# Optimization experiments

Measured on AMD Instinct MI355X. Metric: run time of the kernel, lower is better.

The kernel has to match this reference:

```python
import jax, jax.numpy as jnp
import numpy as np

N_NODES = 50000
N_EDGES = 800000
D_IN = 512
D_OUT = 512


def setup_inputs() -> dict:
    key = jax.random.key(0)
    k1, k2, k3, k4, k5 = jax.random.split(key, 5)
    x = jax.random.normal(k1, (N_NODES, D_IN), dtype=jnp.float32)
    # DGL GraphConv weight: [in_feats, out_feats], xavier-ish scale
    weight = jax.random.normal(k2, (D_IN, D_OUT), dtype=jnp.float32) * (1.0 / np.sqrt(D_IN))
    bias = jax.random.normal(k3, (D_OUT,), dtype=jnp.float32) * 0.01
    src = jax.random.randint(k4, (N_EDGES,), 0, N_NODES, dtype=jnp.int64)
    dst = jax.random.randint(k5, (N_EDGES,), 0, N_NODES, dtype=jnp.int64)
    return {"x": x, "weight": weight, "bias": bias, "src": src, "dst": dst}


def reference(x, weight, bias, src, dst):
    # DGL GraphConv with norm='none': sum messages from src -> dst, then linear.
    # (in_feats == out_feats so DGL aggregates first, then applies W; math is
    # identical either way.)
    msgs = x[src]                                            # [E, D_IN] gather
    agg = jax.ops.segment_sum(msgs, dst, num_segments=N_NODES)  # [N, D_IN]
    return agg @ weight + bias                               # [N, D_OUT]
```

## Files before the change

kernel.cpp:

```cpp
#include <hip/hip_runtime.h>
#include <hip/hip_bf16.h>

#define NN 50000
#define NE 800000
#define DD 512
#define NPAD 50048
#define STRIDE 96

typedef __attribute__((ext_vector_type(8))) short bf16x8;
typedef __attribute__((ext_vector_type(4))) float f32x4;
typedef __attribute__((ext_vector_type(8))) unsigned short u16x8;

__device__ __align__(16) unsigned short g_Wt[DD * DD];
__device__ __align__(16) unsigned short g_xb[(size_t)NN * DD];
__device__ __align__(16) unsigned short g_agg[(size_t)NPAD * DD];
__device__ unsigned g_cnt[NN];
__device__ int g_eidx[(size_t)NN * STRIDE];

static __device__ __forceinline__ unsigned short f2bf(float f) {
    unsigned u = __float_as_uint(f);
    u += 0x7fff + ((u >> 16) & 1);
    return (unsigned short)(u >> 16);
}
static __device__ __forceinline__ float bf2f(unsigned short u) {
    return __uint_as_float((unsigned)u << 16);
}

#define FB_FILL 3125
#define FB_CONV (FB_FILL + 12500)
#define FB_WT   (FB_CONV + 1024)
#define FB_END  (FB_WT + 12)

__global__ void prep_all(const float* __restrict__ x, const float* __restrict__ W,
                         const int* __restrict__ src, const int* __restrict__ dst) {
    int b = blockIdx.x;
    int tid = threadIdx.x;
    if (b < FB_FILL) {
        int i = b * 256 + tid;
        int d = dst[i];
        unsigned pos = atomicAdd(&g_cnt[d], 1u);
        if (pos < STRIDE) g_eidx[(size_t)d * STRIDE + pos] = src[i];
    } else if (b < FB_CONV) {
        size_t base = ((size_t)(b - FB_FILL) * 256 + tid) * 8;
        f32x4 v0 = __builtin_nontemporal_load((const f32x4*)(x + base));
        f32x4 v1 = __builtin_nontemporal_load((const f32x4*)(x + base) + 1);
        u16x8 o;
        o[0] = f2bf(v0[0]); o[1] = f2bf(v0[1]); o[2] = f2bf(v0[2]); o[3] = f2bf(v0[3]);
        o[4] = f2bf(v1[0]); o[5] = f2bf(v1[1]); o[6] = f2bf(v1[2]); o[7] = f2bf(v1[3]);
        *(u16x8*)(g_xb + base) = o;
    } else if (b < FB_WT) {
        int idx = (b - FB_CONV) * 256 + tid;
        int k = idx >> 9, n = idx & 511;
        g_Wt[n * DD + k] = f2bf(W[idx]);
    } else {
        int i = (b - FB_WT) * 256 + tid;
        u16x8 z = {0, 0, 0, 0, 0, 0, 0, 0};
        *(u16x8*)(g_agg + (size_t)NN * DD + (size_t)i * 8) = z;
    }
}

__global__ void aggregate() {
    int v = (blockIdx.x * blockDim.x + threadIdx.x) >> 6;
    int lane = threadIdx.x & 63;
    if (v >= NN) return;
    int deg = (int)g_cnt[v];
    if (deg > STRIDE) deg = STRIDE;
    const int* seg = g_eidx + (size_t)v * STRIDE;
    float a[8] = {0.f, 0.f, 0.f, 0.f, 0.f, 0.f, 0.f, 0.f};
    int i = 0;
    for (; i + 1 < deg; i += 2) {
        int s0 = seg[i], s1 = seg[i + 1];
        int4 q0 = *((const int4*)(g_xb + (size_t)s0 * DD) + lane);
        int4 q1 = *((const int4*)(g_xb + (size_t)s1 * DD) + lane);
        const unsigned short* u0 = (const unsigned short*)&q0;
        const unsigned short* u1 = (const unsigned short*)&q1;
#pragma unroll
        for (int j = 0; j < 8; ++j) a[j] += bf2f(u0[j]) + bf2f(u1[j]);
    }
    if (i < deg) {
        int s0 = seg[i];
        int4 q0 = *((const int4*)(g_xb + (size_t)s0 * DD) + lane);
        const unsigned short* u0 = (const unsigned short*)&q0;
#pragma unroll
        for (int j = 0; j < 8; ++j) a[j] += bf2f(u0[j]);
    }
    u16x8 o;
#pragma unroll
    for (int j = 0; j < 8; ++j) o[j] = f2bf(a[j]);
    *(u16x8*)(g_agg + (size_t)v * DD + lane * 8) = o;
}

#define BM 128
#define BN 128
#define BK 32
#define NWG ((NPAD / BM) * (DD / BN))

__global__ __launch_bounds__(256) void gemm_kernel(float* __restrict__ out,
                                                   const float* __restrict__ bias) {
    __shared__ __align__(16) unsigned short As[BM * BK];
    __shared__ __align__(16) unsigned short Bs[BN * BK];

    const int q = NWG >> 3, r = NWG & 7;
    int xcd = blockIdx.x & 7, sub = blockIdx.x >> 3;
    int swz = (xcd < r) ? xcd * (q + 1) + sub : r * (q + 1) + (xcd - r) * q + sub;
    const int m0 = (swz >> 2) * BM;
    const int n0 = (swz & 3) * BN;

    const int tid = threadIdx.x;
    const int wave = tid >> 6, lane = tid & 63;
    const int wm = wave >> 1, wn = wave & 1;
    const int quad = lane >> 4, l16 = lane & 15;

    const int srow = lane >> 2;
    const int skoff = (lane & 3) * 8;

    f32x4 acc[4][4];
#pragma unroll
    for (int i = 0; i < 4; ++i)
#pragma unroll
        for (int j = 0; j < 4; ++j) acc[i][j] = (f32x4){0.f, 0.f, 0.f, 0.f};

    const unsigned short* gA = g_agg + (size_t)m0 * DD;
    const unsigned short* gB = g_Wt + (size_t)n0 * DD;

    for (int k0 = 0; k0 < DD; k0 += BK) {
#pragma unroll
        for (int is = 0; is < 2; ++is) {
            int row = wave * 32 + is * 16;
            __builtin_amdgcn_global_load_lds(
                (const __attribute__((address_space(1))) void*)
                    (gA + (size_t)(row + srow) * DD + k0 + skoff),
                (__attribute__((address_space(3))) void*)(As + row * BK), 16, 0, 0);
            __builtin_amdgcn_global_load_lds(
                (const __attribute__((address_space(1))) void*)
                    (gB + (size_t)(row + srow) * DD + k0 + skoff),
                (__attribute__((address_space(3))) void*)(Bs + row * BK), 16, 0, 0);
        }
        __syncthreads();

        bf16x8 af[4], bf[4];
#pragma unroll
        for (int t = 0; t < 4; ++t) {
            af[t] = *(const bf16x8*)(&As[(wm * 64 + t * 16 + l16) * BK + quad * 8]);
            bf[t] = *(const bf16x8*)(&Bs[(wn * 64 + t * 16 + l16) * BK + quad * 8]);
        }
#pragma unroll
        for (int am = 0; am < 4; ++am)
#pragma unroll
            for (int bn = 0; bn < 4; ++bn)
                acc[am][bn] = __builtin_amdgcn_mfma_f32_16x16x32_bf16(
                    af[am], bf[bn], acc[am][bn], 0, 0, 0);
        __syncthreads();
    }

#pragma unroll
    for (int am = 0; am < 4; ++am) {
        int row_base = m0 + wm * 64 + am * 16 + quad * 4;
#pragma unroll
        for (int bn = 0; bn < 4; ++bn) {
            int col = n0 + wn * 64 + bn * 16 + l16;
            float bv = bias[col];
#pragma unroll
            for (int rr = 0; rr < 4; ++rr) {
                int rowi = row_base + rr;
                if (rowi < NN) out[(size_t)rowi * DD + col] = acc[am][bn][rr] + bv;
            }
        }
    }
}

extern "C" void kernel_launch(void* const* d_in, const int* in_sizes, int n_in,
                              void* d_out, int out_size, void* d_ws, size_t ws_size,
                              hipStream_t stream) {
    const float* x    = (const float*)d_in[0];
    const float* W    = (const float*)d_in[1];
    const float* bias = (const float*)d_in[2];
    const int*   src  = (const int*)d_in[3];
    const int*   dst  = (const int*)d_in[4];
    float* out = (float*)d_out;
    (void)d_ws; (void)ws_size;

    static void* cnt_ptr = nullptr;
    if (!cnt_ptr) (void)hipGetSymbolAddress(&cnt_ptr, HIP_SYMBOL(g_cnt));
    hipMemsetAsync(cnt_ptr, 0, NN * sizeof(unsigned), stream);

    prep_all<<<FB_END, 256, 0, stream>>>(x, W, src, dst);
    aggregate<<<(NN * 64 + 255) / 256, 256, 0, stream>>>();
    gemm_kernel<<<NWG, 256, 0, stream>>>(out, bias);
}
```

Measured before the change: 406.1 us.

## Double-buffer GEMM LDS tiles and unroll aggregation gather by four

The GEMM now keeps two LDS buffers and issues the global-to-LDS loads for the next K-step before computing on the current one. A single barrier with explicit waitcnts replaces the two __syncthreads per iteration, so load latency can overlap the MFMA work. The aggregation loop also gathers four neighbor rows per iteration instead of two, putting more loads in flight. The cost is doubled LDS use per block, which may lower occupancy, and reliance on hand-placed waitcnts for correctness.

After: 412.6 us. Within noise of the previous version (+1.6%).

```diff
diff --git a/kernel.cpp b/kernel.cpp
--- a/kernel.cpp
+++ b/kernel.cpp
@@ -68,10 +68,24 @@
     const int* seg = g_eidx + (size_t)v * STRIDE;
     float a[8] = {0.f, 0.f, 0.f, 0.f, 0.f, 0.f, 0.f, 0.f};
     int i = 0;
+    for (; i + 3 < deg; i += 4) {
+        int s0 = seg[i], s1 = seg[i + 1], s2 = seg[i + 2], s3 = seg[i + 3];
+        int4 q0 = *((const int4*)(g_xb + ((size_t)s0 << 9)) + lane);
+        int4 q1 = *((const int4*)(g_xb + ((size_t)s1 << 9)) + lane);
+        int4 q2 = *((const int4*)(g_xb + ((size_t)s2 << 9)) + lane);
+        int4 q3 = *((const int4*)(g_xb + ((size_t)s3 << 9)) + lane);
+        const unsigned short* u0 = (const unsigned short*)&q0;
+        const unsigned short* u1 = (const unsigned short*)&q1;
+        const unsigned short* u2 = (const unsigned short*)&q2;
+        const unsigned short* u3 = (const unsigned short*)&q3;
+#pragma unroll
+        for (int j = 0; j < 8; ++j)
+            a[j] += (bf2f(u0[j]) + bf2f(u1[j])) + (bf2f(u2[j]) + bf2f(u3[j]));
+    }
     for (; i + 1 < deg; i += 2) {
         int s0 = seg[i], s1 = seg[i + 1];
-        int4 q0 = *((const int4*)(g_xb + (size_t)s0 * DD) + lane);
-        int4 q1 = *((const int4*)(g_xb + (size_t)s1 * DD) + lane);
+        int4 q0 = *((const int4*)(g_xb + ((size_t)s0 << 9)) + lane);
+        int4 q1 = *((const int4*)(g_xb + ((size_t)s1 << 9)) + lane);
         const unsigned short* u0 = (const unsigned short*)&q0;
         const unsigned short* u1 = (const unsigned short*)&q1;
 #pragma unroll
@@ -79,7 +93,7 @@
     }
     if (i < deg) {
         int s0 = seg[i];
-        int4 q0 = *((const int4*)(g_xb + (size_t)s0 * DD) + lane);
+        int4 q0 = *((const int4*)(g_xb + ((size_t)s0 << 9)) + lane);
         const unsigned short* u0 = (const unsigned short*)&q0;
 #pragma unroll
         for (int j = 0; j < 8; ++j) a[j] += bf2f(u0[j]);
@@ -87,18 +101,19 @@
     u16x8 o;
 #pragma unroll
     for (int j = 0; j < 8; ++j) o[j] = f2bf(a[j]);
-    *(u16x8*)(g_agg + (size_t)v * DD + lane * 8) = o;
+    *(u16x8*)(g_agg + ((size_t)v << 9) + lane * 8) = o;
 }
 
 #define BM 128
 #define BN 128
 #define BK 32
+#define KSTEPS (DD / BK)
 #define NWG ((NPAD / BM) * (DD / BN))
 
 __global__ __launch_bounds__(256) void gemm_kernel(float* __restrict__ out,
                                                    const float* __restrict__ bias) {
-    __shared__ __align__(16) unsigned short As[BM * BK];
-    __shared__ __align__(16) unsigned short Bs[BN * BK];
+    __shared__ __align__(16) unsigned short As[2][BM * BK];
+    __shared__ __align__(16) unsigned short Bs[2][BN * BK];
 
     const int q = NWG >> 3, r = NWG & 7;
     int xcd = blockIdx.x & 7, sub = blockIdx.x >> 3;
@@ -123,35 +138,65 @@
     const unsigned short* gA = g_agg + (size_t)m0 * DD;
     const unsigned short* gB = g_Wt + (size_t)n0 * DD;
 
-    for (int k0 = 0; k0 < DD; k0 += BK) {
-#pragma unroll
-        for (int is = 0; is < 2; ++is) {
-            int row = wave * 32 + is * 16;
-            __builtin_amdgcn_global_load_lds(
-                (const __attribute__((address_space(1))) void*)
-                    (gA + (size_t)(row + srow) * DD + k0 + skoff),
-                (__attribute__((address_space(3))) void*)(As + row * BK), 16, 0, 0);
-            __builtin_amdgcn_global_load_lds(
-                (const __attribute__((address_space(1))) void*)
-                    (gB + (size_t)(row + srow) * DD + k0 + skoff),
-                (__attribute__((address_space(3))) void*)(Bs + row * BK), 16, 0, 0);
+#define STAGE(buf, K0)                                                          \
+    _Pragma("unroll")                                                           \
+    for (int is = 0; is < 2; ++is) {                                            \
+        int row = wave * 32 + is * 16;                                          \
+        __builtin_amdgcn_global_load_lds(                                       \
+            (const __attribute__((address_space(1))) void*)                     \
+                (gA + (size_t)(row + srow) * DD + (K0) + skoff),                \
+            (__attribute__((address_space(3))) void*)(&As[buf][row * BK]), 16, 0, 0); \
+        __builtin_amdgcn_global_load_lds(                                       \
+            (const __attribute__((address_space(1))) void*)                     \
+                (gB + (size_t)(row + srow) * DD + (K0) + skoff),                \
+            (__attribute__((address_space(3))) void*)(&Bs[buf][row * BK]), 16, 0, 0); \
+    }
+
+    STAGE(0, 0)
+    asm volatile("s_waitcnt vmcnt(0)" ::: "memory");
+    __builtin_amdgcn_s_barrier();
+
+    for (int t = 0; t < KSTEPS - 1; ++t) {
+        const int cur = t & 1;
+        STAGE(cur ^ 1, (t + 1) * BK)
+
+        bf16x8 af[4], bf[4];
+#pragma unroll
+        for (int u = 0; u < 4; ++u) {
+            af[u] = *(const bf16x8*)(&As[cur][(wm * 64 + u * 16 + l16) * BK + quad * 8]);
+            bf[u] = *(const bf16x8*)(&Bs[cur][(wn * 64 + u * 16 + l16) * BK + quad * 8]);
         }
-        __syncthreads();
-
-        bf16x8 af[4], bf[4];
-#pragma unroll
-        for (int t = 0; t < 4; ++t) {
-            af[t] = *(const bf16x8*)(&As[(wm * 64 + t * 16 + l16) * BK + quad * 8]);
-            bf[t] = *(const bf16x8*)(&Bs[(wn * 64 + t * 16 + l16) * BK + quad * 8]);
-        }
+        asm volatile("s_waitcnt lgkmcnt(0)" ::: "memory");
+        __builtin_amdgcn_sched_barrier(0);
 #pragma unroll
         for (int am = 0; am < 4; ++am)
 #pragma unroll
             for (int bn = 0; bn < 4; ++bn)
                 acc[am][bn] = __builtin_amdgcn_mfma_f32_16x16x32_bf16(
                     af[am], bf[bn], acc[am][bn], 0, 0, 0);
-        __syncthreads();
-    }
+        asm volatile("s_waitcnt vmcnt(0)" ::: "memory");
+        __builtin_amdgcn_s_barrier();
+        __builtin_amdgcn_sched_barrier(0);
+    }
+
+    {
+        const int cur = (KSTEPS - 1) & 1;
+        bf16x8 af[4], bf[4];
+#pragma unroll
+        for (int u = 0; u < 4; ++u) {
+            af[u] = *(const bf16x8*)(&As[cur][(wm * 64 + u * 16 + l16) * BK + quad * 8]);
+            bf[u] = *(const bf16x8*)(&Bs[cur][(wn * 64 + u * 16 + l16) * BK + quad * 8]);
+        }
+        asm volatile("s_waitcnt lgkmcnt(0)" ::: "memory");
+        __builtin_amdgcn_sched_barrier(0);
+#pragma unroll
+        for (int am = 0; am < 4; ++am)
+#pragma unroll
+            for (int bn = 0; bn < 4; ++bn)
+                acc[am][bn] = __builtin_amdgcn_mfma_f32_16x16x32_bf16(
+                    af[am], bf[bn], acc[am][bn], 0, 0, 0);
+    }
+#undef STAGE
 
 #pragma unroll
     for (int am = 0; am < 4; ++am) {
```

## Transform features before aggregation and fuse edge bucketing into GEMM launch

Applied to the files above, without the earlier changes.

Reorders the computation to apply the weight matrix to node features first (X@W stored as bf16), then gathers and sums the transformed rows per destination node, adding bias and writing fp32 output directly from the aggregation kernel. The edge bucketing (atomic fill) now runs as extra blocks inside the GEMM launch, so it overlaps with the matmul. The gather loop is unrolled by four for more memory-level parallelism. This removes the bf16 aggregate intermediate and the GEMM's fp32 output pass. In exchange it adds a bf16 Y buffer, and the extra bf16 rounding of Y before summation changes numerics.

Result: slower. 418.6 us (+3.1%).

```diff
diff --git a/kernel.cpp b/kernel.cpp
--- a/kernel.cpp
+++ b/kernel.cpp
@@ -12,8 +12,8 @@
 typedef __attribute__((ext_vector_type(8))) unsigned short u16x8;
 
 __device__ __align__(16) unsigned short g_Wt[DD * DD];
-__device__ __align__(16) unsigned short g_xb[(size_t)NN * DD];
-__device__ __align__(16) unsigned short g_agg[(size_t)NPAD * DD];
+__device__ __align__(16) unsigned short g_xb[(size_t)NPAD * DD];
+__device__ __align__(16) unsigned short g_y[(size_t)NPAD * DD];
 __device__ unsigned g_cnt[NN];
 __device__ int g_eidx[(size_t)NN * STRIDE];
 
@@ -26,82 +26,54 @@
     return __uint_as_float((unsigned)u << 16);
 }
 
-#define FB_FILL 3125
-#define FB_CONV (FB_FILL + 12500)
-#define FB_WT   (FB_CONV + 1024)
-#define FB_END  (FB_WT + 12)
-
-__global__ void prep_all(const float* __restrict__ x, const float* __restrict__ W,
-                         const int* __restrict__ src, const int* __restrict__ dst) {
+#define PB_CONV 12500
+#define PB_WT   (PB_CONV + 1024)
+#define PB_END  (PB_WT + 12)
+
+__global__ void prep_xw(const float* __restrict__ x, const float* __restrict__ W) {
     int b = blockIdx.x;
     int tid = threadIdx.x;
-    if (b < FB_FILL) {
-        int i = b * 256 + tid;
-        int d = dst[i];
-        unsigned pos = atomicAdd(&g_cnt[d], 1u);
-        if (pos < STRIDE) g_eidx[(size_t)d * STRIDE + pos] = src[i];
-    } else if (b < FB_CONV) {
-        size_t base = ((size_t)(b - FB_FILL) * 256 + tid) * 8;
+    if (b < PB_CONV) {
+        size_t base = ((size_t)b * 256 + tid) * 8;
         f32x4 v0 = __builtin_nontemporal_load((const f32x4*)(x + base));
         f32x4 v1 = __builtin_nontemporal_load((const f32x4*)(x + base) + 1);
         u16x8 o;
         o[0] = f2bf(v0[0]); o[1] = f2bf(v0[1]); o[2] = f2bf(v0[2]); o[3] = f2bf(v0[3]);
         o[4] = f2bf(v1[0]); o[5] = f2bf(v1[1]); o[6] = f2bf(v1[2]); o[7] = f2bf(v1[3]);
         *(u16x8*)(g_xb + base) = o;
-    } else if (b < FB_WT) {
-        int idx = (b - FB_CONV) * 256 + tid;
+    } else if (b < PB_WT) {
+        int idx = (b - PB_CONV) * 256 + tid;
         int k = idx >> 9, n = idx & 511;
         g_Wt[n * DD + k] = f2bf(W[idx]);
     } else {
-        int i = (b - FB_WT) * 256 + tid;
+        int i = (b - PB_WT) * 256 + tid;
         u16x8 z = {0, 0, 0, 0, 0, 0, 0, 0};
-        *(u16x8*)(g_agg + (size_t)NN * DD + (size_t)i * 8) = z;
-    }
-}
-
-__global__ void aggregate() {
-    int v = (blockIdx.x * blockDim.x + threadIdx.x) >> 6;
-    int lane = threadIdx.x & 63;
-    if (v >= NN) return;
-    int deg = (int)g_cnt[v];
-    if (deg > STRIDE) deg = STRIDE;
-    const int* seg = g_eidx + (size_t)v * STRIDE;
-    float a[8] = {0.f, 0.f, 0.f, 0.f, 0.f, 0.f, 0.f, 0.f};
-    int i = 0;
-    for (; i + 1 < deg; i += 2) {
-        int s0 = seg[i], s1 = seg[i + 1];
-        int4 q0 = *((const int4*)(g_xb + (size_t)s0 * DD) + lane);
-        int4 q1 = *((const int4*)(g_xb + (size_t)s1 * DD) + lane);
-        const unsigned short* u0 = (const unsigned short*)&q0;
-        const unsigned short* u1 = (const unsigned short*)&q1;
-#pragma unroll
-        for (int j = 0; j < 8; ++j) a[j] += bf2f(u0[j]) + bf2f(u1[j]);
-    }
-    if (i < deg) {
-        int s0 = seg[i];
-        int4 q0 = *((const int4*)(g_xb + (size_t)s0 * DD) + lane);
-        const unsigned short* u0 = (const unsigned short*)&q0;
-#pragma unroll
-        for (int j = 0; j < 8; ++j) a[j] += bf2f(u0[j]);
-    }
-    u16x8 o;
-#pragma unroll
-    for (int j = 0; j < 8; ++j) o[j] = f2bf(a[j]);
-    *(u16x8*)(g_agg + (size_t)v * DD + lane * 8) = o;
+        *(u16x8*)(g_xb + (size_t)NN * DD + (size_t)i * 8) = z;
+    }
 }
 
 #define BM 128
 #define BN 128
 #define BK 32
 #define NWG ((NPAD / BM) * (DD / BN))
-
-__global__ __launch_bounds__(256) void gemm_kernel(float* __restrict__ out,
-                                                   const float* __restrict__ bias) {
+#define FG_FILL 3125
+#define FG_END  (FG_FILL + NWG)
+
+__global__ __launch_bounds__(256) void fill_gemm(const int* __restrict__ src,
+                                                 const int* __restrict__ dst) {
+    if (blockIdx.x < FG_FILL) {
+        int i = blockIdx.x * 256 + threadIdx.x;
+        int d = dst[i];
+        unsigned pos = atomicAdd(&g_cnt[d], 1u);
+        if (pos < STRIDE) g_eidx[(size_t)d * STRIDE + pos] = src[i];
+        return;
+    }
     __shared__ __align__(16) unsigned short As[BM * BK];
     __shared__ __align__(16) unsigned short Bs[BN * BK];
 
+    const int bid = blockIdx.x - FG_FILL;
     const int q = NWG >> 3, r = NWG & 7;
-    int xcd = blockIdx.x & 7, sub = blockIdx.x >> 3;
+    int xcd = bid & 7, sub = bid >> 3;
     int swz = (xcd < r) ? xcd * (q + 1) + sub : r * (q + 1) + (xcd - r) * q + sub;
     const int m0 = (swz >> 2) * BM;
     const int n0 = (swz & 3) * BN;
@@ -120,7 +92,7 @@
 #pragma unroll
         for (int j = 0; j < 4; ++j) acc[i][j] = (f32x4){0.f, 0.f, 0.f, 0.f};
 
-    const unsigned short* gA = g_agg + (size_t)m0 * DD;
+    const unsigned short* gA = g_xb + (size_t)m0 * DD;
     const unsigned short* gB = g_Wt + (size_t)n0 * DD;
 
     for (int k0 = 0; k0 < DD; k0 += BK) {
@@ -159,14 +131,59 @@
 #pragma unroll
         for (int bn = 0; bn < 4; ++bn) {
             int col = n0 + wn * 64 + bn * 16 + l16;
-            float bv = bias[col];
-#pragma unroll
-            for (int rr = 0; rr < 4; ++rr) {
-                int rowi = row_base + rr;
-                if (rowi < NN) out[(size_t)rowi * DD + col] = acc[am][bn][rr] + bv;
-            }
+#pragma unroll
+            for (int rr = 0; rr < 4; ++rr)
+                g_y[(size_t)(row_base + rr) * DD + col] = f2bf(acc[am][bn][rr]);
         }
     }
+}
+
+__global__ void aggregate(float* __restrict__ out, const float* __restrict__ bias) {
+    int v = (blockIdx.x * blockDim.x + threadIdx.x) >> 6;
+    int lane = threadIdx.x & 63;
+    if (v >= NN) return;
+    int deg = (int)g_cnt[v];
+    if (deg > STRIDE) deg = STRIDE;
+    const int* seg = g_eidx + (size_t)v * STRIDE;
+    float a[8] = {0.f, 0.f, 0.f, 0.f, 0.f, 0.f, 0.f, 0.f};
+    int i = 0;
+    for (; i + 3 < deg; i += 4) {
+        int s0 = seg[i], s1 = seg[i + 1], s2 = seg[i + 2], s3 = seg[i + 3];
+        int4 q0 = *((const int4*)(g_y + ((size_t)s0 << 9)) + lane);
+        int4 q1 = *((const int4*)(g_y + ((size_t)s1 << 9)) + lane);
+        int4 q2 = *((const int4*)(g_y + ((size_t)s2 << 9)) + lane);
+        int4 q3 = *((const int4*)(g_y + ((size_t)s3 << 9)) + lane);
+        const unsigned short* u0 = (const unsigned short*)&q0;
+        const unsigned short* u1 = (const unsigned short*)&q1;
+        const unsigned short* u2 = (const unsigned short*)&q2;
+        const unsigned short* u3 = (const unsigned short*)&q3;
+#pragma unroll
+        for (int j = 0; j < 8; ++j)
+            a[j] += (bf2f(u0[j]) + bf2f(u1[j])) + (bf2f(u2[j]) + bf2f(u3[j]));
+    }
+    for (; i + 1 < deg; i += 2) {
+        int s0 = seg[i], s1 = seg[i + 1];
+        int4 q0 = *((const int4*)(g_y + ((size_t)s0 << 9)) + lane);
+        int4 q1 = *((const int4*)(g_y + ((size_t)s1 << 9)) + lane);
+        const unsigned short* u0 = (const unsigned short*)&q0;
+        const unsigned short* u1 = (const unsigned short*)&q1;
+#pragma unroll
+        for (int j = 0; j < 8; ++j) a[j] += bf2f(u0[j]) + bf2f(u1[j]);
+    }
+    if (i < deg) {
+        int s0 = seg[i];
+        int4 q0 = *((const int4*)(g_y + ((size_t)s0 << 9)) + lane);
+        const unsigned short* u0 = (const unsigned short*)&q0;
+#pragma unroll
+        for (int j = 0; j < 8; ++j) a[j] += bf2f(u0[j]);
+    }
+    f32x4 b0 = *(const f32x4*)(bias + lane * 8);
+    f32x4 b1 = *(const f32x4*)(bias + lane * 8 + 4);
+    f32x4 o0 = {a[0] + b0[0], a[1] + b0[1], a[2] + b0[2], a[3] + b0[3]};
+    f32x4 o1 = {a[4] + b1[0], a[5] + b1[1], a[6] + b1[2], a[7] + b1[3]};
+    float* op = out + ((size_t)v << 9) + lane * 8;
+    *(f32x4*)op = o0;
+    *(f32x4*)(op + 4) = o1;
 }
 
 extern "C" void kernel_launch(void* const* d_in, const int* in_sizes, int n_in,
@@ -184,7 +201,7 @@
     if (!cnt_ptr) (void)hipGetSymbolAddress(&cnt_ptr, HIP_SYMBOL(g_cnt));
     hipMemsetAsync(cnt_ptr, 0, NN * sizeof(unsigned), stream);
 
-    prep_all<<<FB_END, 256, 0, stream>>>(x, W, src, dst);
-    aggregate<<<(NN * 64 + 255) / 256, 256, 0, stream>>>();
-    gemm_kernel<<<NWG, 256, 0, stream>>>(out, bias);
-}
+    prep_xw<<<PB_END, 256, 0, stream>>>(x, W);
+    fill_gemm<<<FG_END, 256, 0, stream>>>(src, dst);
+    aggregate<<<(NN * 64 + 255) / 256, 256, 0, stream>>>(out, bias);
+}
```

## Split aggregation into column slices and source-node halves for cache locality

Applied to the files above, without the earlier changes.

The aggregate kernel now gives each block one of eight 64-column slices for 16 destination nodes, and each lane reads one bf16 element per edge instead of 16 bytes. It also walks the edge list twice, handling only sources in one half of the node range per pass. Both aim to shrink the working set of gathered x rows so they stay in L2/MALL cache. The cost is many more narrow 2-byte loads, eight times more reads of the index list, and two passes of branching per edge, with scalar stores in place of vector stores.

Result: slower. 881.0 us (+116.9%).

```diff
diff --git a/kernel.cpp b/kernel.cpp
--- a/kernel.cpp
+++ b/kernel.cpp
@@ -59,35 +59,32 @@
     }
 }
 
-__global__ void aggregate() {
-    int v = (blockIdx.x * blockDim.x + threadIdx.x) >> 6;
-    int lane = threadIdx.x & 63;
-    if (v >= NN) return;
+__global__ __launch_bounds__(1024) void aggregate() {
+    const int slice = blockIdx.x & 7;
+    const int chunk = blockIdx.x >> 3;
+    const int lane = threadIdx.x & 63;
+    const int v = chunk * 16 + (threadIdx.x >> 6);
     int deg = (int)g_cnt[v];
     if (deg > STRIDE) deg = STRIDE;
     const int* seg = g_eidx + (size_t)v * STRIDE;
-    float a[8] = {0.f, 0.f, 0.f, 0.f, 0.f, 0.f, 0.f, 0.f};
-    int i = 0;
-    for (; i + 1 < deg; i += 2) {
-        int s0 = seg[i], s1 = seg[i + 1];
-        int4 q0 = *((const int4*)(g_xb + (size_t)s0 * DD) + lane);
-        int4 q1 = *((const int4*)(g_xb + (size_t)s1 * DD) + lane);
-        const unsigned short* u0 = (const unsigned short*)&q0;
-        const unsigned short* u1 = (const unsigned short*)&q1;
-#pragma unroll
-        for (int j = 0; j < 8; ++j) a[j] += bf2f(u0[j]) + bf2f(u1[j]);
+    const unsigned short* xs = g_xb + (slice << 6) + lane;
+    float a0 = 0.f, a1 = 0.f, a2 = 0.f, a3 = 0.f;
+    for (int h = 0; h < 2; ++h) {
+        const int lo = h * (NN / 2), hi = lo + (NN / 2);
+        int i = 0;
+        for (; i + 3 < deg; i += 4) {
+            int s0 = seg[i], s1 = seg[i + 1], s2 = seg[i + 2], s3 = seg[i + 3];
+            if (s0 >= lo && s0 < hi) a0 += bf2f(xs[(size_t)s0 << 9]);
+            if (s1 >= lo && s1 < hi) a1 += bf2f(xs[(size_t)s1 << 9]);
+            if (s2 >= lo && s2 < hi) a2 += bf2f(xs[(size_t)s2 << 9]);
+            if (s3 >= lo && s3 < hi) a3 += bf2f(xs[(size_t)s3 << 9]);
+        }
+        for (; i < deg; ++i) {
+            int s0 = seg[i];
+            if (s0 >= lo && s0 < hi) a0 += bf2f(xs[(size_t)s0 << 9]);
+        }
     }
-    if (i < deg) {
-        int s0 = seg[i];
-        int4 q0 = *((const int4*)(g_xb + (size_t)s0 * DD) + lane);
-        const unsigned short* u0 = (const unsigned short*)&q0;
-#pragma unroll
-        for (int j = 0; j < 8; ++j) a[j] += bf2f(u0[j]);
-    }
-    u16x8 o;
-#pragma unroll
-    for (int j = 0; j < 8; ++j) o[j] = f2bf(a[j]);
-    *(u16x8*)(g_agg + (size_t)v * DD + lane * 8) = o;
+    g_agg[((size_t)v << 9) + (slice << 6) + lane] = f2bf((a0 + a1) + (a2 + a3));
 }
 
 #define BM 128
@@ -185,6 +182,6 @@
     hipMemsetAsync(cnt_ptr, 0, NN * sizeof(unsigned), stream);
 
     prep_all<<<FB_END, 256, 0, stream>>>(x, W, src, dst);
-    aggregate<<<(NN * 64 + 255) / 256, 256, 0, stream>>>();
+    aggregate<<<3125 * 8, 1024, 0, stream>>>();
     gemm_kernel<<<NWG, 256, 0, stream>>>(out, bias);
 }
```
